# Performance work log

Measured on AMD Instinct MI355X. Metric: run time of the kernel, lower is better.

Reference implementation:

```python
import jax, jax.numpy as jnp
import numpy as np

N = 50000
E = 800000
IN_C, HID, OUT_C, HEADS = 128, 32, 64, 4
NEG_SLOPE = 0.2


def setup_inputs() -> dict:
    key = jax.random.key(0)
    ks = jax.random.split(key, 10)
    x = jax.random.normal(ks[0], (N, IN_C), dtype=jnp.float32)
    edge_index = jax.random.randint(ks[1], (2, E), 0, N, dtype=jnp.int64)
    s = 0.05
    W1 = jax.random.normal(ks[2], (IN_C, HID), dtype=jnp.float32) * s
    b1 = jnp.zeros((HID,), dtype=jnp.float32)
    Wg = jax.random.normal(ks[3], (HID, HEADS * HID), dtype=jnp.float32) * s
    ag_src = jax.random.normal(ks[4], (HEADS, HID), dtype=jnp.float32) * s
    ag_dst = jax.random.normal(ks[5], (HEADS, HID), dtype=jnp.float32) * s
    bg = jnp.zeros((HID,), dtype=jnp.float32)
    W2 = jax.random.normal(ks[6], (HID, OUT_C), dtype=jnp.float32) * s
    b2 = jnp.zeros((OUT_C,), dtype=jnp.float32)
    return {"x": x, "edge_index": edge_index, "W1": W1, "b1": b1,
            "Wg": Wg, "ag_src": ag_src, "ag_dst": ag_dst, "bg": bg,
            "W2": W2, "b2": b2}


def _add_self_loops(edge_index, n):
    loop = jnp.arange(n, dtype=edge_index.dtype)
    return jnp.concatenate([edge_index, jnp.stack([loop, loop])], axis=1)


def _gcn(x, src, dst, W, b, n):
    # PyG GCNConv: symmetric normalization with self-loops, scatter-add
    xw = x @ W  # [N, F]
    deg = jnp.zeros((n,), xw.dtype).at[dst].add(1.0)  # in-degree incl self-loops
    dinv = jax.lax.rsqrt(deg)
    norm = dinv[src] * dinv[dst]  # [E']
    msg = xw[src] * norm[:, None]  # [E', F]
    out = jax.ops.segment_sum(msg, dst, num_segments=n)
    return out + b


def _gat(x, src, dst, Wg, a_src, a_dst, b, n):
    # PyG GATConv, concat=False (mean over heads), leaky_relu slope 0.2
    h = (x @ Wg).reshape(n, HEADS, HID)  # [N, H, D]
    al_s = jnp.einsum('nhd,hd->nh', h, a_src)  # [N, H]
    al_d = jnp.einsum('nhd,hd->nh', h, a_dst)
    logits = jax.nn.leaky_relu(al_s[src] + al_d[dst], NEG_SLOPE)  # [E', H]
    # segment softmax over incoming edges of each dst node
    m = jax.ops.segment_max(logits, dst, num_segments=n)
    e = jnp.exp(logits - m[dst])
    denom = jax.ops.segment_sum(e, dst, num_segments=n)
    alpha = e / denom[dst]  # [E', H]
    msg = h[src] * alpha[:, :, None]  # [E', H, D]
    out = jax.ops.segment_sum(msg, dst, num_segments=n)  # [N, H, D]
    return out.mean(axis=1) + b


def reference(x, edge_index, W1, b1, Wg, ag_src, ag_dst, bg, W2, b2):
    ei = _add_self_loops(edge_index, N)
    src, dst = ei[0], ei[1]
    h = jax.nn.relu(_gcn(x, src, dst, W1, b1, N))
    h = jax.nn.relu(_gat(h, src, dst, Wg, ag_src, ag_dst, bg, N))
    return _gcn(h, src, dst, W2, b2, N)
```

## Files before the change

kernel.cpp:

```cpp
#include <hip/hip_runtime.h>
#include <hip/hip_bf16.h>

#define N_NODES 50000
#define N_EDGES 800000
#define IN_C 128
#define HID 32
#define OUT_C 64
#define HEADS 4
#define NEG_SLOPE 0.2f

#define MAXDEG 64

typedef unsigned int uint32;
typedef __attribute__((ext_vector_type(8))) short bf16x8;
typedef __attribute__((ext_vector_type(4))) float f32x4;

__device__ __forceinline__ float bf_lo(uint32 u) { return __uint_as_float(u << 16); }
__device__ __forceinline__ float bf_hi(uint32 u) { return __uint_as_float(u & 0xffff0000u); }
__device__ __forceinline__ uint32 f2bf(float f) {
    uint32 u = __float_as_uint(f);
    return (u + 0x7fffu + ((u >> 16) & 1u)) >> 16;
}
__device__ __forceinline__ uint32 pack_bf2(float a, float b) {
    return f2bf(a) | (f2bf(b) << 16);
}

__global__ __launch_bounds__(256) void k_scatter(const int* __restrict__ ei,
                                                 int* __restrict__ ncnt,
                                                 int* __restrict__ srcs_pad,
                                                 const float* __restrict__ Wg,
                                                 const float* __restrict__ ags,
                                                 const float* __restrict__ agd,
                                                 float* __restrict__ wals,
                                                 float* __restrict__ wald,
                                                 const float* __restrict__ W2,
                                                 uint32* __restrict__ wgB,
                                                 uint32* __restrict__ w2B) {
    int t = threadIdx.x;
    int e = blockIdx.x * 256 + t;
    if (e < N_EDGES) {
        int s = ei[e];
        int d = ei[N_EDGES + e];
        int pos = atomicAdd(&ncnt[d], 1);
        if (pos < MAXDEG) srcs_pad[(d << 6) + pos] = s;
    }
    if (blockIdx.x == 0) {
        {
            int c = t & 127;
            int h = c >> 5, k = c & 31;
            const float* a = (t < 128) ? ags : agd;
            float acc = 0.f;
#pragma unroll
            for (int d = 0; d < 32; d++) acc += Wg[k * 128 + h * 32 + d] * a[h * 32 + d];
            if (t < 128) wals[c] = acc; else wald[c] = acc;
        }
        for (int i = t; i < 2048; i += 256) {
            int tile = i >> 8;
            int T = tile >> 2, kt = tile & 3;
            int r = i & 255;
            int L = r >> 2, di = r & 3;
            int k0 = kt * 32 + (L >> 4) * 8 + 2 * di;
            int k1 = k0 + 1;
            int n = T * 16 + (L & 15);
            float a = Wg[(k0 & 31) * 128 + (k0 >> 5) * 32 + n];
            float b = Wg[(k1 & 31) * 128 + (k1 >> 5) * 32 + n];
            wgB[i] = pack_bf2(a, b);
        }
        for (int i = t; i < 1024; i += 256) {
            int T = i >> 8;
            int r = i & 255;
            int L = r >> 2, di = r & 3;
            int k0 = (L >> 4) * 8 + 2 * di;
            int n = T * 16 + (L & 15);
            w2B[i] = pack_bf2(W2[k0 * 64 + n], W2[(k0 + 1) * 64 + n]);
        }
    }
}

__global__ __launch_bounds__(256) void k_gemm1(const float* __restrict__ x,
                                               const float* __restrict__ W1,
                                               const int* __restrict__ ncnt,
                                               uint32* __restrict__ xw1) {
    __shared__ float wl[IN_C * HID];
    __shared__ float xl[8 * IN_C];
    int t = threadIdx.x;
    for (int i = t; i < IN_C * HID; i += 256) {
        int k = i >> 5, f = i & 31;
        wl[(k >> 1) * 64 + f * 2 + (k & 1)] = W1[i];
    }
    int nb = blockIdx.x * 8;
    const float4* x4 = (const float4*)(x + (size_t)nb * IN_C);
    ((float4*)xl)[t] = x4[t];
    __syncthreads();
    int g = t >> 5, f = t & 31;
    const float2* xr = (const float2*)(xl + g * IN_C);
    const float2* wp = (const float2*)wl;
    float acc = 0.f;
#pragma unroll 16
    for (int k2 = 0; k2 < 64; k2++) {
        float2 xv = xr[k2];
        float2 wv = wp[k2 * 32 + f];
        acc += xv.x * wv.x + xv.y * wv.y;
    }
    float v = acc * rsqrtf((float)(ncnt[nb + g] + 1));
    float vn = __shfl_xor(v, 1, 64);
    if ((f & 1) == 0) xw1[(size_t)(nb + g) * 16 + (f >> 1)] = pack_bf2(v, vn);
}

__global__ __launch_bounds__(256) void k_gather1(const uint32* __restrict__ xw1,
                                                 const int* __restrict__ ncnt,
                                                 const int* __restrict__ srcs_pad,
                                                 const float* __restrict__ b1,
                                                 const float* __restrict__ wals,
                                                 const float* __restrict__ wald,
                                                 char* __restrict__ recH,
                                                 float* __restrict__ als,
                                                 float* __restrict__ ald) {
    int t = threadIdx.x;
    int l16 = t & 15;
    int es = l16 >> 2;
    int q  = l16 & 3;
    int n = blockIdx.x * 16 + (t >> 4);
    int deg = ncnt[n];
    float a0 = 0.f, a1 = 0.f, a2 = 0.f, a3 = 0.f;
    float a4 = 0.f, a5 = 0.f, a6 = 0.f, a7 = 0.f;
#pragma unroll 2
    for (int jb = 0; jb <= deg; jb += 4) {
        int je = jb + es;
        if (je <= deg) {
            int sidx = (je < deg) ? srcs_pad[(n << 6) + je] : n;
            uint4 u = *(const uint4*)((const char*)xw1 + ((uint32)sidx << 6) + q * 16);
            a0 += bf_lo(u.x); a1 += bf_hi(u.x);
            a2 += bf_lo(u.y); a3 += bf_hi(u.y);
            a4 += bf_lo(u.z); a5 += bf_hi(u.z);
            a6 += bf_lo(u.w); a7 += bf_hi(u.w);
        }
    }
#define RED_ES(v) v += __shfl_xor(v, 4, 64); v += __shfl_xor(v, 8, 64);
    RED_ES(a0) RED_ES(a1) RED_ES(a2) RED_ES(a3)
    RED_ES(a4) RED_ES(a5) RED_ES(a6) RED_ES(a7)
#undef RED_ES
    float dn = rsqrtf((float)(deg + 1));
    float4 bA = ((const float4*)b1)[2 * q];
    float4 bB = ((const float4*)b1)[2 * q + 1];
    float v0 = a0 * dn + bA.x, v1 = a1 * dn + bA.y;
    float v2 = a2 * dn + bA.z, v3 = a3 * dn + bA.w;
    float v4 = a4 * dn + bB.x, v5 = a5 * dn + bB.y;
    float v6 = a6 * dn + bB.z, v7 = a7 * dn + bB.w;
    v0 = v0 > 0.f ? v0 : 0.f; v1 = v1 > 0.f ? v1 : 0.f;
    v2 = v2 > 0.f ? v2 : 0.f; v3 = v3 > 0.f ? v3 : 0.f;
    v4 = v4 > 0.f ? v4 : 0.f; v5 = v5 > 0.f ? v5 : 0.f;
    v6 = v6 > 0.f ? v6 : 0.f; v7 = v7 > 0.f ? v7 : 0.f;
    if (es == 0) {
        uint4 w;
        w.x = pack_bf2(v0, v1); w.y = pack_bf2(v2, v3);
        w.z = pack_bf2(v4, v5); w.w = pack_bf2(v6, v7);
        *(uint4*)(recH + ((uint32)n << 6) + q * 16) = w;
    }
    float ps[4], pd[4];
#pragma unroll
    for (int h = 0; h < 4; h++) {
        const float4* wa = (const float4*)(wals + h * 32 + 8 * q);
        float4 wv0 = wa[0], wv1 = wa[1];
        ps[h] = v0 * wv0.x + v1 * wv0.y + v2 * wv0.z + v3 * wv0.w
              + v4 * wv1.x + v5 * wv1.y + v6 * wv1.z + v7 * wv1.w;
        const float4* wb = (const float4*)(wald + h * 32 + 8 * q);
        float4 uv0 = wb[0], uv1 = wb[1];
        pd[h] = v0 * uv0.x + v1 * uv0.y + v2 * uv0.z + v3 * uv0.w
              + v4 * uv1.x + v5 * uv1.y + v6 * uv1.z + v7 * uv1.w;
    }
#pragma unroll
    for (int h = 0; h < 4; h++) {
        ps[h] += __shfl_xor(ps[h], 1, 64); ps[h] += __shfl_xor(ps[h], 2, 64);
        pd[h] += __shfl_xor(pd[h], 1, 64); pd[h] += __shfl_xor(pd[h], 2, 64);
    }
    if (l16 == 0) {
        ((float4*)als)[n] = make_float4(ps[0], ps[1], ps[2], ps[3]);
        ((float4*)ald)[n] = make_float4(pd[0], pd[1], pd[2], pd[3]);
    }
}

__global__ __launch_bounds__(512) void k_gat_agg(const char* __restrict__ recH,
                                                 const float* __restrict__ als,
                                                 const float* __restrict__ ald,
                                                 const int* __restrict__ ncnt,
                                                 const int* __restrict__ srcs_pad,
                                                 const uint32* __restrict__ wgB,
                                                 const float* __restrict__ bg,
                                                 uint32* __restrict__ h2s) {
    __shared__ __align__(16) uint32 gl[16][64];
    int t = threadIdx.x;
    int l32 = t & 31;
    int g8 = t >> 5;
    int n = blockIdx.x * 16 + g8;
    int es = l32 >> 3;
    int q  = l32 & 7;
    int deg = ncnt[n];
    float4 dv = ((const float4*)ald)[n];

    float g00 = 0.f, g01 = 0.f, g02 = 0.f, g03 = 0.f;
    float g10 = 0.f, g11 = 0.f, g12 = 0.f, g13 = 0.f;
    float g20 = 0.f, g21 = 0.f, g22 = 0.f, g23 = 0.f;
    float g30 = 0.f, g31 = 0.f, g32 = 0.f, g33 = 0.f;
    float ss0 = 0.f, ss1 = 0.f, ss2 = 0.f, ss3 = 0.f;

#pragma unroll 2
    for (int jb = 0; jb <= deg; jb += 4) {
        int je = jb + es;
        if (je <= deg) {
            int sidx = (je < deg) ? srcs_pad[(n << 6) + je] : n;
            float4 ev = ((const float4*)als)[sidx];
            uint2 u = *(const uint2*)(recH + ((uint32)sidx << 6) + q * 8);
            float f0 = bf_lo(u.x), f1 = bf_hi(u.x);
            float f2 = bf_lo(u.y), f3 = bf_hi(u.y);
            float tt, w;
            tt = ev.x + dv.x; w = __expf(fmaxf(tt, NEG_SLOPE * tt));
            ss0 += w; g00 += w * f0; g01 += w * f1; g02 += w * f2; g03 += w * f3;
            tt = ev.y + dv.y; w = __expf(fmaxf(tt, NEG_SLOPE * tt));
            ss1 += w; g10 += w * f0; g11 += w * f1; g12 += w * f2; g13 += w * f3;
            tt = ev.z + dv.z; w = __expf(fmaxf(tt, NEG_SLOPE * tt));
            ss2 += w; g20 += w * f0; g21 += w * f1; g22 += w * f2; g23 += w * f3;
            tt = ev.w + dv.w; w = __expf(fmaxf(tt, NEG_SLOPE * tt));
            ss3 += w; g30 += w * f0; g31 += w * f1; g32 += w * f2; g33 += w * f3;
        }
    }
#define RED_ES(v) v += __shfl_xor(v, 8, 64); v += __shfl_xor(v, 16, 64);
    RED_ES(ss0) RED_ES(ss1) RED_ES(ss2) RED_ES(ss3)
    RED_ES(g00) RED_ES(g01) RED_ES(g02) RED_ES(g03)
    RED_ES(g10) RED_ES(g11) RED_ES(g12) RED_ES(g13)
    RED_ES(g20) RED_ES(g21) RED_ES(g22) RED_ES(g23)
    RED_ES(g30) RED_ES(g31) RED_ES(g32) RED_ES(g33)
#undef RED_ES
    float i0 = 0.25f / ss0, i1 = 0.25f / ss1, i2 = 0.25f / ss2, i3 = 0.25f / ss3;
    if (es == 0) {
        uint2 w;
        w.x = pack_bf2(g00 * i0, g01 * i0); w.y = pack_bf2(g02 * i0, g03 * i0);
        *(uint2*)&gl[g8][0 * 16 + 2 * q] = w;
        w.x = pack_bf2(g10 * i1, g11 * i1); w.y = pack_bf2(g12 * i1, g13 * i1);
        *(uint2*)&gl[g8][1 * 16 + 2 * q] = w;
        w.x = pack_bf2(g20 * i2, g21 * i2); w.y = pack_bf2(g22 * i2, g23 * i2);
        *(uint2*)&gl[g8][2 * 16 + 2 * q] = w;
        w.x = pack_bf2(g30 * i3, g31 * i3); w.y = pack_bf2(g32 * i3, g33 * i3);
        *(uint2*)&gl[g8][3 * 16 + 2 * q] = w;
    }
    __syncthreads();
    if (t < 64) {
        int L = t;
        int mA = L & 15;
        int quad = L >> 4;
        int nbase = blockIdx.x * 16;
        float dns[4];
#pragma unroll
        for (int r = 0; r < 4; r++)
            dns[r] = rsqrtf((float)(ncnt[nbase + quad * 4 + r] + 1));
#pragma unroll
        for (int T = 0; T < 2; T++) {
            f32x4 acc = {0.f, 0.f, 0.f, 0.f};
#pragma unroll
            for (int kt = 0; kt < 4; kt++) {
                bf16x8 af = *(const bf16x8*)&gl[mA][kt * 16 + quad * 4];
                bf16x8 bf = *(const bf16x8*)(wgB + (size_t)((T * 4 + kt) * 64 + L) * 4);
                acc = __builtin_amdgcn_mfma_f32_16x16x32_bf16(af, bf, acc, 0, 0, 0);
            }
            int d = T * 16 + (L & 15);
            float bgd = bg[d];
#pragma unroll
            for (int r = 0; r < 4; r++) {
                int node = nbase + quad * 4 + r;
                float v = acc[r] + bgd;
                v = v > 0.f ? v : 0.f;
                v *= dns[r];
                float vn = __shfl_xor(v, 1, 64);
                if ((d & 1) == 0)
                    h2s[(size_t)node * 16 + (d >> 1)] = pack_bf2(v, vn);
            }
        }
    }
}

__global__ __launch_bounds__(256) void k_gather2(const uint32* __restrict__ h2s,
                                                 const int* __restrict__ ncnt,
                                                 const int* __restrict__ srcs_pad,
                                                 const uint32* __restrict__ w2B,
                                                 const float* __restrict__ b2,
                                                 float* __restrict__ out) {
    __shared__ __align__(16) uint32 gbf[16][16];
    int t = threadIdx.x;
    int l16 = t & 15;
    int es = l16 >> 2;
    int q  = l16 & 3;
    int g16 = t >> 4;
    int n = blockIdx.x * 16 + g16;
    int deg = ncnt[n];
    float a0 = 0.f, a1 = 0.f, a2 = 0.f, a3 = 0.f;
    float a4 = 0.f, a5 = 0.f, a6 = 0.f, a7 = 0.f;
#pragma unroll 2
    for (int jb = 0; jb <= deg; jb += 4) {
        int je = jb + es;
        if (je <= deg) {
            int sidx = (je < deg) ? srcs_pad[(n << 6) + je] : n;
            uint4 u = *(const uint4*)((const char*)h2s + ((uint32)sidx << 6) + q * 16);
            a0 += bf_lo(u.x); a1 += bf_hi(u.x);
            a2 += bf_lo(u.y); a3 += bf_hi(u.y);
            a4 += bf_lo(u.z); a5 += bf_hi(u.z);
            a6 += bf_lo(u.w); a7 += bf_hi(u.w);
        }
    }
#define RED_ES(v) v += __shfl_xor(v, 4, 64); v += __shfl_xor(v, 8, 64);
    RED_ES(a0) RED_ES(a1) RED_ES(a2) RED_ES(a3)
    RED_ES(a4) RED_ES(a5) RED_ES(a6) RED_ES(a7)
#undef RED_ES
    if (es == 0) {
        uint4 w;
        w.x = pack_bf2(a0, a1); w.y = pack_bf2(a2, a3);
        w.z = pack_bf2(a4, a5); w.w = pack_bf2(a6, a7);
        *(uint4*)&gbf[g16][4 * q] = w;
    }
    __syncthreads();
    if (t < 64) {
        int L = t;
        int quad = L >> 4;
        int nbase = blockIdx.x * 16;
        float dns[4];
#pragma unroll
        for (int r = 0; r < 4; r++)
            dns[r] = rsqrtf((float)(ncnt[nbase + quad * 4 + r] + 1));
        bf16x8 af = *(const bf16x8*)&gbf[L & 15][quad * 4];
#pragma unroll
        for (int T = 0; T < 4; T++) {
            bf16x8 bf = *(const bf16x8*)(w2B + (size_t)(T * 64 + L) * 4);
            f32x4 acc = {0.f, 0.f, 0.f, 0.f};
            acc = __builtin_amdgcn_mfma_f32_16x16x32_bf16(af, bf, acc, 0, 0, 0);
            int d = T * 16 + (L & 15);
            float b2d = b2[d];
#pragma unroll
            for (int r = 0; r < 4; r++) {
                int node = nbase + quad * 4 + r;
                out[(size_t)node * OUT_C + d] = acc[r] * dns[r] + b2d;
            }
        }
    }
}

extern "C" void kernel_launch(void* const* d_in, const int* in_sizes, int n_in,
                              void* d_out, int out_size, void* d_ws, size_t ws_size,
                              hipStream_t stream) {
    const float* x   = (const float*)d_in[0];
    const int*   ei  = (const int*)d_in[1];
    const float* W1  = (const float*)d_in[2];
    const float* b1  = (const float*)d_in[3];
    const float* Wg  = (const float*)d_in[4];
    const float* ags = (const float*)d_in[5];
    const float* agd = (const float*)d_in[6];
    const float* bg  = (const float*)d_in[7];
    const float* W2  = (const float*)d_in[8];
    const float* b2  = (const float*)d_in[9];
    float* out = (float*)d_out;

    char* p = (char*)d_ws;
    auto alloc = [&](size_t bytes) -> void* {
        void* r = (void*)p;
        p += (bytes + 255) & ~(size_t)255;
        return r;
    };
    int*    ncnt     = (int*)  alloc((size_t)N_NODES * 4);
    int*    srcs_pad = (int*)  alloc((size_t)N_NODES * MAXDEG * 4);
    uint32* xw1      = (uint32*)alloc((size_t)N_NODES * 16 * 4);
    char*   recH     = (char*) alloc((size_t)N_NODES * 64);
    float*  als      = (float*)alloc((size_t)N_NODES * 4 * 4);
    float*  ald      = (float*)alloc((size_t)N_NODES * 4 * 4);
    float*  wals     = (float*)alloc(128 * 4);
    float*  wald     = (float*)alloc(128 * 4);
    uint32* wgB      = (uint32*)alloc(2048 * 4);
    uint32* w2B      = (uint32*)alloc(1024 * 4);
    uint32* h2s      = (uint32*)alloc((size_t)N_NODES * 16 * 4);

    hipMemsetAsync(ncnt, 0, (size_t)N_NODES * 4, stream);

    k_scatter<<<(N_EDGES + 255) / 256, 256, 0, stream>>>(
        ei, ncnt, srcs_pad, Wg, ags, agd, wals, wald, W2, wgB, w2B);

    k_gemm1<<<N_NODES / 8, 256, 0, stream>>>(x, W1, ncnt, xw1);

    k_gather1<<<N_NODES / 16, 256, 0, stream>>>(xw1, ncnt, srcs_pad, b1,
                                                wals, wald, recH, als, ald);

    k_gat_agg<<<N_NODES / 16, 512, 0, stream>>>(recH, als, ald, ncnt, srcs_pad,
                                                wgB, bg, h2s);

    k_gather2<<<N_NODES / 16, 256, 0, stream>>>(h2s, ncnt, srcs_pad, w2B, b2, out);
}
```

Baseline: 227.7 us.

## Store neighbor lists as 16-bit indices and bin scatter atomics by node range

Shrinks the padded source-index table from 32-bit to 16-bit entries, halving the bytes read by the three gather kernels and written by the scatter. The scatter kernel now runs 2048 blocks, each thread handling two edges. It performs atomics in four destination-range passes separated by block barriers, so that concurrent scattered writes stay within a smaller region for better cache locality. Node ids up to 50000 fit in an unsigned short. The extra passes, barriers and branches add overhead to the scatter.

```diff
diff --git a/kernel.cpp b/kernel.cpp
--- a/kernel.cpp
+++ b/kernel.cpp
@@ -10,8 +10,13 @@
 #define NEG_SLOPE 0.2f
 
 #define MAXDEG 64
+#define SC_BLOCKS 2048
+#define SC_G (SC_BLOCKS * 256)
+#define N_PASS 4
+#define PASS_W ((N_NODES + N_PASS - 1) / N_PASS)
 
 typedef unsigned int uint32;
+typedef unsigned short ushort16;
 typedef __attribute__((ext_vector_type(8))) short bf16x8;
 typedef __attribute__((ext_vector_type(4))) float f32x4;
 
@@ -27,7 +32,7 @@
 
 __global__ __launch_bounds__(256) void k_scatter(const int* __restrict__ ei,
                                                  int* __restrict__ ncnt,
-                                                 int* __restrict__ srcs_pad,
+                                                 ushort16* __restrict__ srcs_pad,
                                                  const float* __restrict__ Wg,
                                                  const float* __restrict__ ags,
                                                  const float* __restrict__ agd,
@@ -37,12 +42,22 @@
                                                  uint32* __restrict__ wgB,
                                                  uint32* __restrict__ w2B) {
     int t = threadIdx.x;
-    int e = blockIdx.x * 256 + t;
-    if (e < N_EDGES) {
-        int s = ei[e];
-        int d = ei[N_EDGES + e];
-        int pos = atomicAdd(&ncnt[d], 1);
-        if (pos < MAXDEG) srcs_pad[(d << 6) + pos] = s;
+    int gid = blockIdx.x * 256 + t;
+    int s0 = 0, d0 = -1, s1 = 0, d1 = -1;
+    if (gid < N_EDGES)        { s0 = ei[gid];        d0 = ei[N_EDGES + gid]; }
+    if (gid + SC_G < N_EDGES) { s1 = ei[gid + SC_G]; d1 = ei[N_EDGES + gid + SC_G]; }
+#pragma unroll
+    for (int p = 0; p < N_PASS; p++) {
+        int lo = p * PASS_W, hi = lo + PASS_W;
+        if (d0 >= lo && d0 < hi) {
+            int pos = atomicAdd(&ncnt[d0], 1);
+            if (pos < MAXDEG) srcs_pad[(d0 << 6) + pos] = (ushort16)s0;
+        }
+        if (d1 >= lo && d1 < hi) {
+            int pos = atomicAdd(&ncnt[d1], 1);
+            if (pos < MAXDEG) srcs_pad[(d1 << 6) + pos] = (ushort16)s1;
+        }
+        __syncthreads();
     }
     if (blockIdx.x == 0) {
         {
@@ -109,7 +124,7 @@
 
 __global__ __launch_bounds__(256) void k_gather1(const uint32* __restrict__ xw1,
                                                  const int* __restrict__ ncnt,
-                                                 const int* __restrict__ srcs_pad,
+                                                 const ushort16* __restrict__ srcs_pad,
                                                  const float* __restrict__ b1,
                                                  const float* __restrict__ wals,
                                                  const float* __restrict__ wald,
@@ -128,7 +143,7 @@
     for (int jb = 0; jb <= deg; jb += 4) {
         int je = jb + es;
         if (je <= deg) {
-            int sidx = (je < deg) ? srcs_pad[(n << 6) + je] : n;
+            int sidx = (je < deg) ? (int)srcs_pad[(n << 6) + je] : n;
             uint4 u = *(const uint4*)((const char*)xw1 + ((uint32)sidx << 6) + q * 16);
             a0 += bf_lo(u.x); a1 += bf_hi(u.x);
             a2 += bf_lo(u.y); a3 += bf_hi(u.y);
@@ -184,7 +199,7 @@
                                                  const float* __restrict__ als,
                                                  const float* __restrict__ ald,
                                                  const int* __restrict__ ncnt,
-                                                 const int* __restrict__ srcs_pad,
+                                                 const ushort16* __restrict__ srcs_pad,
                                                  const uint32* __restrict__ wgB,
                                                  const float* __restrict__ bg,
                                                  uint32* __restrict__ h2s) {
@@ -208,7 +223,7 @@
     for (int jb = 0; jb <= deg; jb += 4) {
         int je = jb + es;
         if (je <= deg) {
-            int sidx = (je < deg) ? srcs_pad[(n << 6) + je] : n;
+            int sidx = (je < deg) ? (int)srcs_pad[(n << 6) + je] : n;
             float4 ev = ((const float4*)als)[sidx];
             uint2 u = *(const uint2*)(recH + ((uint32)sidx << 6) + q * 8);
             float f0 = bf_lo(u.x), f1 = bf_hi(u.x);
@@ -280,7 +295,7 @@
 
 __global__ __launch_bounds__(256) void k_gather2(const uint32* __restrict__ h2s,
                                                  const int* __restrict__ ncnt,
-                                                 const int* __restrict__ srcs_pad,
+                                                 const ushort16* __restrict__ srcs_pad,
                                                  const uint32* __restrict__ w2B,
                                                  const float* __restrict__ b2,
                                                  float* __restrict__ out) {
@@ -298,7 +313,7 @@
     for (int jb = 0; jb <= deg; jb += 4) {
         int je = jb + es;
         if (je <= deg) {
-            int sidx = (je < deg) ? srcs_pad[(n << 6) + je] : n;
+            int sidx = (je < deg) ? (int)srcs_pad[(n << 6) + je] : n;
             uint4 u = *(const uint4*)((const char*)h2s + ((uint32)sidx << 6) + q * 16);
             a0 += bf_lo(u.x); a1 += bf_hi(u.x);
             a2 += bf_lo(u.y); a3 += bf_hi(u.y);
@@ -363,21 +378,21 @@
         p += (bytes + 255) & ~(size_t)255;
         return r;
     };
-    int*    ncnt     = (int*)  alloc((size_t)N_NODES * 4);
-    int*    srcs_pad = (int*)  alloc((size_t)N_NODES * MAXDEG * 4);
-    uint32* xw1      = (uint32*)alloc((size_t)N_NODES * 16 * 4);
-    char*   recH     = (char*) alloc((size_t)N_NODES * 64);
-    float*  als      = (float*)alloc((size_t)N_NODES * 4 * 4);
-    float*  ald      = (float*)alloc((size_t)N_NODES * 4 * 4);
-    float*  wals     = (float*)alloc(128 * 4);
-    float*  wald     = (float*)alloc(128 * 4);
-    uint32* wgB      = (uint32*)alloc(2048 * 4);
-    uint32* w2B      = (uint32*)alloc(1024 * 4);
-    uint32* h2s      = (uint32*)alloc((size_t)N_NODES * 16 * 4);
+    int*      ncnt     = (int*)    alloc((size_t)N_NODES * 4);
+    ushort16* srcs_pad = (ushort16*)alloc((size_t)N_NODES * MAXDEG * 2);
+    uint32*   xw1      = (uint32*) alloc((size_t)N_NODES * 16 * 4);
+    char*     recH     = (char*)   alloc((size_t)N_NODES * 64);
+    float*    als      = (float*)  alloc((size_t)N_NODES * 4 * 4);
+    float*    ald      = (float*)  alloc((size_t)N_NODES * 4 * 4);
+    float*    wals     = (float*)  alloc(128 * 4);
+    float*    wald     = (float*)  alloc(128 * 4);
+    uint32*   wgB      = (uint32*) alloc(2048 * 4);
+    uint32*   w2B      = (uint32*) alloc(1024 * 4);
+    uint32*   h2s      = (uint32*) alloc((size_t)N_NODES * 16 * 4);
 
     hipMemsetAsync(ncnt, 0, (size_t)N_NODES * 4, stream);
 
-    k_scatter<<<(N_EDGES + 255) / 256, 256, 0, stream>>>(
+    k_scatter<<<SC_BLOCKS, 256, 0, stream>>>(
         ei, ncnt, srcs_pad, Wg, ags, agd, wals, wald, W2, wgB, w2B);
 
     k_gemm1<<<N_NODES / 8, 256, 0, stream>>>(x, W1, ncnt, xw1);
```

Result: faster. 222.9 us (-2.1%).
